# Performance work log

Hardware: AMD Instinct MI355X
Metric: run time of the kernel (lower is better)

The kernel has to match this reference:

```python
import jax, jax.numpy as jnp
import numpy as np

N_NODES = 100000
N_EDGES = 1600000
F_IN = 128
HEADS1, CH1 = 8, 16
N_CLASSES = 64
NEG_SLOPE = 0.2  # PyG GATConv default leaky-relu slope


def setup_inputs() -> dict:
    key = jax.random.key(0)
    ks = jax.random.split(key, 10)
    x = jax.random.normal(ks[0], (N_NODES, F_IN), dtype=jnp.float32)
    edge_index = jax.random.randint(ks[1], (2, N_EDGES), 0, N_NODES, dtype=jnp.int32)
    s1 = 1.0 / np.sqrt(F_IN)
    s2 = 1.0 / np.sqrt(HEADS1 * CH1)
    W1 = jax.random.normal(ks[2], (F_IN, HEADS1 * CH1), dtype=jnp.float32) * s1
    a_src1 = jax.random.normal(ks[3], (HEADS1, CH1), dtype=jnp.float32) * s2
    a_dst1 = jax.random.normal(ks[4], (HEADS1, CH1), dtype=jnp.float32) * s2
    b1 = jnp.zeros((HEADS1 * CH1,), dtype=jnp.float32)
    W2 = jax.random.normal(ks[5], (HEADS1 * CH1, N_CLASSES), dtype=jnp.float32) * s2
    a_src2 = jax.random.normal(ks[6], (1, N_CLASSES), dtype=jnp.float32) * 0.1
    a_dst2 = jax.random.normal(ks[7], (1, N_CLASSES), dtype=jnp.float32) * 0.1
    b2 = jnp.zeros((N_CLASSES,), dtype=jnp.float32)
    return {"x": x, "edge_index": edge_index, "W1": W1, "a_src1": a_src1,
            "a_dst1": a_dst1, "b1": b1, "W2": W2, "a_src2": a_src2,
            "a_dst2": a_dst2, "b2": b2}


def gat_layer(x, src, dst, W, a_src, a_dst, b, heads, ch, concat):
    # PyG GATConv (eval mode, self-loops already appended to src/dst).
    N = x.shape[0]
    h = (x @ W).reshape(N, heads, ch)                      # [N,H,C]
    asn = jnp.einsum('nhc,hc->nh', h, a_src)               # src attention term
    adn = jnp.einsum('nhc,hc->nh', h, a_dst)               # dst attention term
    e = jax.nn.leaky_relu(asn[src] + adn[dst], NEG_SLOPE)  # [E,H]
    emax = jax.ops.segment_max(e, dst, num_segments=N)     # per-dst max (self-loops guarantee nonempty)
    ee = jnp.exp(e - emax[dst])
    denom = jax.ops.segment_sum(ee, dst, num_segments=N)
    alpha = ee / denom[dst]                                # segment softmax over incoming edges
    msg = h[src] * alpha[:, :, None]                       # [E,H,C]
    out = jax.ops.segment_sum(msg, dst, num_segments=N)    # [N,H,C]
    out = out.reshape(N, heads * ch) if concat else out.mean(axis=1)
    return out + b


def reference(x, edge_index, W1, a_src1, a_dst1, b1, W2, a_src2, a_dst2, b2):
    N = x.shape[0]
    loop = jnp.arange(N, dtype=edge_index.dtype)
    src = jnp.concatenate([edge_index[0], loop])  # add self-loops (PyG default)
    dst = jnp.concatenate([edge_index[1], loop])
    h = gat_layer(x, src, dst, W1, a_src1, a_dst1, b1, HEADS1, CH1, True)
    h = jax.nn.elu(h)
    # F.dropout with training=False is identity (eval mode)
    out = gat_layer(h, src, dst, W2, a_src2, a_dst2, b2, 1, N_CLASSES, False)
    return jax.nn.log_softmax(out, axis=1)
```

## Files before the change

kernel.cpp:

```cpp
#include <hip/hip_runtime.h>

#define NN 100000
#define NE 1600000
#define EN (NE + NN)
#define FIN 128
#define H1 8
#define C1 16
#define F1 128
#define NC 64
#define NEG 0.2f

#define BSH 9
#define BKN 512
#define NBUK ((NN + BKN - 1) / BKN)
#define NBLK 256
#define CHUNK ((EN + NBLK - 1) / NBLK)

typedef unsigned short ushort_t;
typedef unsigned int uint_t;
typedef __attribute__((ext_vector_type(8))) short short8v;
typedef __attribute__((ext_vector_type(4))) float f32x4;
typedef __attribute__((ext_vector_type(2))) float f32x2;

union U8 { ushort_t u[8]; short8v v; uint4 q; };

__device__ __forceinline__ ushort_t f2bf(float f) {
  uint_t u = __builtin_bit_cast(uint_t, f);
  u += 0x7FFF + ((u >> 16) & 1);
  return (ushort_t)(u >> 16);
}
__device__ __forceinline__ float bflo(uint_t u) {
  return __builtin_bit_cast(float, u << 16);
}
__device__ __forceinline__ float bfhi(uint_t u) {
  return __builtin_bit_cast(float, u & 0xFFFF0000u);
}

#if __has_builtin(__builtin_amdgcn_cvt_pk_fp8_f32) && \
    __has_builtin(__builtin_amdgcn_cvt_pk_f32_fp8)
__device__ __forceinline__ uint_t fp8_pack4(float f0, float f1, float f2,
                                            float f3) {
  int p = 0;
  p = __builtin_amdgcn_cvt_pk_fp8_f32(f0, f1, p, false);
  p = __builtin_amdgcn_cvt_pk_fp8_f32(f2, f3, p, true);
  return (uint_t)p;
}
__device__ __forceinline__ void fp8_unpack4(uint_t w, float* o) {
  f32x2 d0 = __builtin_amdgcn_cvt_pk_f32_fp8((int)w, false);
  f32x2 d1 = __builtin_amdgcn_cvt_pk_f32_fp8((int)w, true);
  o[0] = d0.x; o[1] = d0.y; o[2] = d1.x; o[3] = d1.y;
}
#else
__device__ __forceinline__ uint_t fp8_enc1(float f) {
  uint_t u = __builtin_bit_cast(uint_t, f);
  uint_t s = (u >> 24) & 0x80u;
  int e = (int)((u >> 23) & 0xFF) - 127;
  if (e < -9) return s;
  if (e < -6) {
    float af = __builtin_bit_cast(float, u & 0x7FFFFFFFu);
    uint_t m = (uint_t)(af * 512.f + 0.5f);
    return s | m;
  }
  uint_t mant = u & 0x7FFFFF;
  uint_t keep = mant >> 20;
  uint_t rest = mant & 0xFFFFF;
  keep += (rest > 0x80000u) || (rest == 0x80000u && (keep & 1));
  uint_t ee = (uint_t)(e + 7);
  if (keep == 8) { keep = 0; ee += 1; }
  if (ee > 15 || (ee == 15 && keep > 6)) return s | 0x7E;
  return s | (ee << 3) | keep;
}
__device__ __forceinline__ float fp8_dec1(uint_t b) {
  uint_t s = (b & 0x80u) << 24;
  uint_t e = (b >> 3) & 15u, m = b & 7u;
  if (e == 0) {
    float v = (float)m * (1.0f / 512.0f);
    return __builtin_bit_cast(float, s | __builtin_bit_cast(uint_t, v));
  }
  return __builtin_bit_cast(float, s | ((e + 120u) << 23) | (m << 20));
}
__device__ __forceinline__ uint_t fp8_pack4(float f0, float f1, float f2,
                                            float f3) {
  return fp8_enc1(f0) | (fp8_enc1(f1) << 8) | (fp8_enc1(f2) << 16) |
         (fp8_enc1(f3) << 24);
}
__device__ __forceinline__ void fp8_unpack4(uint_t w, float* o) {
  o[0] = fp8_dec1(w & 0xFF); o[1] = fp8_dec1((w >> 8) & 0xFF);
  o[2] = fp8_dec1((w >> 16) & 0xFF); o[3] = fp8_dec1(w >> 24);
}
#endif

__global__ __launch_bounds__(256) void mfma_gemm1_kernel(
    const float* __restrict__ X, const ushort_t* __restrict__ WT1,
    const float* __restrict__ a_src, const float* __restrict__ a_dst,
    uint2* __restrict__ h8, float* __restrict__ asn, float* __restrict__ adn,
    int nrows) {
  const int tid = threadIdx.x;
  const int wave = tid >> 6, lane = tid & 63;
  const int row0 = blockIdx.x * 64 + wave * 16;
  const int rlo = lane & 15, khi = lane >> 4;

  f32x4 acc[8];
#pragma unroll
  for (int n = 0; n < 8; ++n) acc[n] = (f32x4){0.f, 0.f, 0.f, 0.f};

#pragma unroll
  for (int ks = 0; ks < 4; ++ks) {
    const int kk = ks * 32 + khi * 8;
    int row = row0 + rlo;
    if (row >= nrows) row = nrows - 1;
    const float4* xp = (const float4*)(X + (size_t)row * 128 + kk);
    float4 u = xp[0], v = xp[1];
    U8 t;
    t.u[0] = f2bf(u.x); t.u[1] = f2bf(u.y); t.u[2] = f2bf(u.z); t.u[3] = f2bf(u.w);
    t.u[4] = f2bf(v.x); t.u[5] = f2bf(v.y); t.u[6] = f2bf(v.z); t.u[7] = f2bf(v.w);
    short8v a = t.v;
#pragma unroll
    for (int nf = 0; nf < 8; ++nf) {
      short8v b = *(const short8v*)(WT1 + (nf * 16 + rlo) * 128 + kk);
      acc[nf] = __builtin_amdgcn_mfma_f32_16x16x32_bf16(a, b, acc[nf], 0, 0, 0);
    }
  }
  const float4* as4 = (const float4*)a_src;
  const float4* ad4 = (const float4*)a_dst;
  float4 as0 = as4[rlo * 2], as1 = as4[rlo * 2 + 1];
  float4 ad0 = ad4[rlo * 2], ad1 = ad4[rlo * 2 + 1];
  int rbase = row0 + khi * 4;
#pragma unroll
  for (int r = 0; r < 4; ++r) {
    int row = rbase + r;
    bool ok = (row < nrows);
    uint2 pk;
    pk.x = fp8_pack4(acc[0][r], acc[1][r], acc[2][r], acc[3][r]);
    pk.y = fp8_pack4(acc[4][r], acc[5][r], acc[6][r], acc[7][r]);
    if (ok) h8[(size_t)row * 16 + rlo] = pk;
    float s = acc[0][r] * as0.x + acc[1][r] * as0.y +
              acc[2][r] * as0.z + acc[3][r] * as0.w +
              acc[4][r] * as1.x + acc[5][r] * as1.y +
              acc[6][r] * as1.z + acc[7][r] * as1.w;
    float d = acc[0][r] * ad0.x + acc[1][r] * ad0.y +
              acc[2][r] * ad0.z + acc[3][r] * ad0.w +
              acc[4][r] * ad1.x + acc[5][r] * ad1.y +
              acc[6][r] * ad1.z + acc[7][r] * ad1.w;
    s += __shfl_xor(s, 1);
    d += __shfl_xor(d, 1);
    if (ok && (rlo & 1) == 0) {
      asn[row * 8 + (rlo >> 1)] = s;
      adn[row * 8 + (rlo >> 1)] = d;
    }
  }
}

__global__ __launch_bounds__(256) void mfma_gemm2_kernel(
    const ushort_t* __restrict__ X2, const ushort_t* __restrict__ WT2,
    const float* __restrict__ a_src, const float* __restrict__ a_dst,
    uint_t* __restrict__ h28, float* __restrict__ asn, float* __restrict__ adn,
    int nrows) {
  const int tid = threadIdx.x;
  const int wave = tid >> 6, lane = tid & 63;
  const int row0 = blockIdx.x * 64 + wave * 16;
  const int rlo = lane & 15, khi = lane >> 4;

  f32x4 acc[4];
#pragma unroll
  for (int n = 0; n < 4; ++n) acc[n] = (f32x4){0.f, 0.f, 0.f, 0.f};

#pragma unroll
  for (int ks = 0; ks < 4; ++ks) {
    const int kk = ks * 32 + khi * 8;
    int row = row0 + rlo;
    if (row >= nrows) row = nrows - 1;
    U8 t;
    t.q = *(const uint4*)(X2 + (size_t)row * 128 + kk);
    short8v a = t.v;
#pragma unroll
    for (int nf = 0; nf < 4; ++nf) {
      short8v b = *(const short8v*)(WT2 + (nf * 16 + rlo) * 128 + kk);
      acc[nf] = __builtin_amdgcn_mfma_f32_16x16x32_bf16(a, b, acc[nf], 0, 0, 0);
    }
  }
  float4 as = ((const float4*)a_src)[rlo];
  float4 ad = ((const float4*)a_dst)[rlo];
  int rbase = row0 + khi * 4;
#pragma unroll
  for (int r = 0; r < 4; ++r) {
    int row = rbase + r;
    bool ok = (row < nrows);
    uint_t pk = fp8_pack4(acc[0][r], acc[1][r], acc[2][r], acc[3][r]);
    if (ok) h28[(size_t)row * 16 + rlo] = pk;
    float s = acc[0][r] * as.x + acc[1][r] * as.y +
              acc[2][r] * as.z + acc[3][r] * as.w;
    float d = acc[0][r] * ad.x + acc[1][r] * ad.y +
              acc[2][r] * ad.z + acc[3][r] * ad.w;
    s += __shfl_xor(s, 1); s += __shfl_xor(s, 2);
    s += __shfl_xor(s, 4); s += __shfl_xor(s, 8);
    d += __shfl_xor(d, 1); d += __shfl_xor(d, 2);
    d += __shfl_xor(d, 4); d += __shfl_xor(d, 8);
    if (ok && rlo == 0) { asn[row] = s; adn[row] = d; }
  }
}

__global__ __launch_bounds__(512) void bucket_count_kernel(
    const int* __restrict__ dstA, int* __restrict__ cnt,
    const float* __restrict__ W1, const float* __restrict__ W2,
    ushort_t* __restrict__ WT1, ushort_t* __restrict__ WT2) {
  __shared__ int histL[NBUK];
  int b = blockIdx.x, t = threadIdx.x;
  int gid = b * 512 + t;
  if (gid < 128 * 128) {
    int n = gid >> 7, k = gid & 127;
    int c = (n & 15) * 8 + (n >> 4);
    WT1[gid] = f2bf(W1[k * 128 + c]);
  } else if (gid < 128 * 128 + 64 * 128) {
    int j = gid - 128 * 128;
    int n = j >> 7, k = j & 127;
    int c = (n & 15) * 4 + (n >> 4);
    WT2[j] = f2bf(W2[k * 64 + c]);
  }
  for (int i = t; i < NBUK; i += 512) histL[i] = 0;
  __syncthreads();
  int e0 = b * CHUNK, e1 = min(e0 + CHUNK, EN);
  for (int e = e0 + t; e < e1; e += 512) {
    int d = (e < NE) ? dstA[e] : (e - NE);
    atomicAdd(&histL[d >> BSH], 1);
  }
  __syncthreads();
  for (int i = t; i < NBUK; i += 512) cnt[i * NBLK + b] = histL[i];
}

__global__ __launch_bounds__(256) void bucket_scan_kernel(
    int* __restrict__ cnt, int* __restrict__ bucket_base) {
  __shared__ int colsum[NBUK];
  int t = threadIdx.x;
  if (t < NBUK) {
    int run = 0;
    int* c = cnt + t * NBLK;
    for (int b = 0; b < NBLK; ++b) { int v = c[b]; c[b] = run; run += v; }
    colsum[t] = run;
  }
  __syncthreads();
  if (t == 0) {
    int base = 0;
    for (int j = 0; j < NBUK; ++j) {
      bucket_base[j] = base;
      int v = colsum[j];
      colsum[j] = base;
      base += v;
    }
    bucket_base[NBUK] = base;
  }
  __syncthreads();
  if (t < NBUK) {
    int bb = colsum[t];
    int* c = cnt + t * NBLK;
    for (int b = 0; b < NBLK; ++b) c[b] += bb;
  }
}

__global__ __launch_bounds__(512) void bucket_scatter_kernel(
    const int* __restrict__ srcA, const int* __restrict__ dstA,
    const int* __restrict__ cnt, int* __restrict__ staging) {
  __shared__ int cur[NBUK];
  int b = blockIdx.x, t = threadIdx.x;
  for (int i = t; i < NBUK; i += 512) cur[i] = cnt[i * NBLK + b];
  __syncthreads();
  int e0 = b * CHUNK, e1 = min(e0 + CHUNK, EN);
  for (int e = e0 + t; e < e1; e += 512) {
    int s, d;
    if (e < NE) { s = srcA[e]; d = dstA[e]; } else { s = e - NE; d = s; }
    int pos = atomicAdd(&cur[d >> BSH], 1);
    staging[pos] = s | ((d & (BKN - 1)) << 17);
  }
}

__global__ __launch_bounds__(512) void bucket_csr_kernel(
    const int* __restrict__ staging, const int* __restrict__ bucket_base,
    int* __restrict__ rp, int* __restrict__ col) {
  __shared__ int degL[BKN];
  __shared__ int exclL[BKN];
  __shared__ int sdata[2][BKN];
  int bk = blockIdx.x, t = threadIdx.x;
  int ebase = bucket_base[bk], eend = bucket_base[bk + 1];
  int ecnt = eend - ebase;
  degL[t] = 0;
  __syncthreads();
  for (int e = t; e < ecnt; e += 512)
    atomicAdd(&degL[staging[ebase + e] >> 17], 1);
  __syncthreads();
  int v = degL[t];
  sdata[0][t] = v;
  __syncthreads();
  int sp = 0;
  for (int off = 1; off < BKN; off <<= 1) {
    int val = sdata[sp][t];
    if (t >= off) val += sdata[sp][t - off];
    sdata[sp ^ 1][t] = val;
    __syncthreads();
    sp ^= 1;
  }
  int ex = sdata[sp][t] - v;
  exclL[t] = ex;
  int node = bk * BKN + t;
  if (node < NN) rp[node] = ebase + ex;
  if (bk == 0 && t == 0) rp[NN] = EN;
  __syncthreads();
  for (int e = t; e < ecnt; e += 512) {
    int pk = staging[ebase + e];
    int pos = atomicAdd(&exclL[pk >> 17], 1);
    col[ebase + pos] = pk & 0x1FFFF;
  }
}

__global__ __launch_bounds__(256) void gather1_kernel(
    const int* __restrict__ rp, const int* __restrict__ col,
    const float* __restrict__ asn, const float* __restrict__ adn,
    const uint4* __restrict__ h8, const float* __restrict__ b1,
    ushort_t* __restrict__ x2) {
  int node = (blockIdx.x << 5) + (threadIdx.x >> 3);
  if (node >= NN) return;
  int lane = threadIdx.x & 7;
  float aD = adn[node * 8 + lane];
  int p = rp[node], p1 = rp[node + 1];
  float a[16];
#pragma unroll
  for (int j = 0; j < 16; ++j) a[j] = 0.f;
  float den = 0.f;

  for (; p + 1 < p1; p += 2) {
    int s0 = col[p], s1 = col[p + 1];
    float e0 = asn[s0 * 8 + lane] + aD;
    float e1 = asn[s1 * 8 + lane] + aD;
    uint4 q0 = h8[(size_t)s0 * 8 + lane];
    uint4 q1 = h8[(size_t)s1 * 8 + lane];
    e0 = e0 > 0.f ? e0 : NEG * e0;
    e1 = e1 > 0.f ? e1 : NEG * e1;
    float ee0 = __expf(e0), ee1 = __expf(e1);
    float d0[4], d1[4], d2[4], d3[4];
    fp8_unpack4(q0.x, d0); fp8_unpack4(q0.y, d1);
    fp8_unpack4(q0.z, d2); fp8_unpack4(q0.w, d3);
    float g0[4], g1[4], g2[4], g3[4];
    fp8_unpack4(q1.x, g0); fp8_unpack4(q1.y, g1);
    fp8_unpack4(q1.z, g2); fp8_unpack4(q1.w, g3);
#pragma unroll
    for (int j = 0; j < 4; ++j) {
      a[j]      += ee0 * d0[j] + ee1 * g0[j];
      a[4 + j]  += ee0 * d1[j] + ee1 * g1[j];
      a[8 + j]  += ee0 * d2[j] + ee1 * g2[j];
      a[12 + j] += ee0 * d3[j] + ee1 * g3[j];
    }
    den += ee0 + ee1;
  }
  if (p < p1) {
    int s0 = col[p];
    float e0 = asn[s0 * 8 + lane] + aD;
    uint4 q0 = h8[(size_t)s0 * 8 + lane];
    e0 = e0 > 0.f ? e0 : NEG * e0;
    float ee0 = __expf(e0);
    float d0[4], d1[4], d2[4], d3[4];
    fp8_unpack4(q0.x, d0); fp8_unpack4(q0.y, d1);
    fp8_unpack4(q0.z, d2); fp8_unpack4(q0.w, d3);
#pragma unroll
    for (int j = 0; j < 4; ++j) {
      a[j] += ee0 * d0[j];
      a[4 + j] += ee0 * d1[j];
      a[8 + j] += ee0 * d2[j];
      a[12 + j] += ee0 * d3[j];
    }
    den += ee0;
  }
  float inv = 1.f / den;
  const float4* b4 = (const float4*)b1;
  U8 t0, t1;
#pragma unroll
  for (int h = 0; h < 4; ++h) {
    float4 bv = b4[lane * 4 + h];
    float o0 = fmaf(a[h * 4 + 0], inv, bv.x);
    float o1 = fmaf(a[h * 4 + 1], inv, bv.y);
    float o2 = fmaf(a[h * 4 + 2], inv, bv.z);
    float o3 = fmaf(a[h * 4 + 3], inv, bv.w);
    o0 = o0 > 0.f ? o0 : __expf(o0) - 1.f;
    o1 = o1 > 0.f ? o1 : __expf(o1) - 1.f;
    o2 = o2 > 0.f ? o2 : __expf(o2) - 1.f;
    o3 = o3 > 0.f ? o3 : __expf(o3) - 1.f;
    U8& t = (h < 2) ? t0 : t1;
    int base = (h & 1) * 4;
    t.u[base + 0] = f2bf(o0); t.u[base + 1] = f2bf(o1);
    t.u[base + 2] = f2bf(o2); t.u[base + 3] = f2bf(o3);
  }
  uint4* xr = (uint4*)(x2 + (size_t)node * F1);
  xr[lane * 2 + 0] = t0.q;
  xr[lane * 2 + 1] = t1.q;
}

__global__ __launch_bounds__(256) void gather2_kernel(
    const int* __restrict__ rp, const int* __restrict__ col,
    const float* __restrict__ asn, const float* __restrict__ adn,
    const uint2* __restrict__ h28, const float* __restrict__ b2,
    float* __restrict__ out) {
  int node = (blockIdx.x << 5) + (threadIdx.x >> 3);
  if (node >= NN) return;
  int lane = threadIdx.x & 7;
  float aD = adn[node];
  int p = rp[node], p1 = rp[node + 1];
  float a[8];
#pragma unroll
  for (int j = 0; j < 8; ++j) a[j] = 0.f;
  float den = 0.f;

  for (; p + 1 < p1; p += 2) {
    int s0 = col[p], s1 = col[p + 1];
    float e0 = asn[s0] + aD;
    float e1 = asn[s1] + aD;
    uint2 q0 = h28[(size_t)s0 * 8 + lane];
    uint2 q1 = h28[(size_t)s1 * 8 + lane];
    e0 = e0 > 0.f ? e0 : NEG * e0;
    e1 = e1 > 0.f ? e1 : NEG * e1;
    float ee0 = __expf(e0), ee1 = __expf(e1);
    float d0[4], d1[4], g0[4], g1[4];
    fp8_unpack4(q0.x, d0); fp8_unpack4(q0.y, d1);
    fp8_unpack4(q1.x, g0); fp8_unpack4(q1.y, g1);
#pragma unroll
    for (int j = 0; j < 4; ++j) {
      a[j] += ee0 * d0[j] + ee1 * g0[j];
      a[4 + j] += ee0 * d1[j] + ee1 * g1[j];
    }
    den += ee0 + ee1;
  }
  if (p < p1) {
    int s0 = col[p];
    float e0 = asn[s0] + aD;
    uint2 q0 = h28[(size_t)s0 * 8 + lane];
    e0 = e0 > 0.f ? e0 : NEG * e0;
    float ee0 = __expf(e0);
    float d0[4], d1[4];
    fp8_unpack4(q0.x, d0); fp8_unpack4(q0.y, d1);
#pragma unroll
    for (int j = 0; j < 4; ++j) {
      a[j] += ee0 * d0[j];
      a[4 + j] += ee0 * d1[j];
    }
    den += ee0;
  }
  float inv = 1.f / den;
  float4 bv0 = ((const float4*)b2)[lane * 2 + 0];
  float4 bv1 = ((const float4*)b2)[lane * 2 + 1];
  float v[8];
  v[0] = fmaf(a[0], inv, bv0.x); v[1] = fmaf(a[1], inv, bv0.y);
  v[2] = fmaf(a[2], inv, bv0.z); v[3] = fmaf(a[3], inv, bv0.w);
  v[4] = fmaf(a[4], inv, bv1.x); v[5] = fmaf(a[5], inv, bv1.y);
  v[6] = fmaf(a[6], inv, bv1.z); v[7] = fmaf(a[7], inv, bv1.w);
  float m = v[0];
#pragma unroll
  for (int j = 1; j < 8; ++j) m = fmaxf(m, v[j]);
#pragma unroll
  for (int k = 1; k < 8; k <<= 1) m = fmaxf(m, __shfl_xor(m, k));
  float ex = 0.f;
#pragma unroll
  for (int j = 0; j < 8; ++j) ex += __expf(v[j] - m);
#pragma unroll
  for (int k = 1; k < 8; k <<= 1) ex += __shfl_xor(ex, k);
  float lse = m + __logf(ex);
  float4 r0 = {v[0] - lse, v[1] - lse, v[2] - lse, v[3] - lse};
  float4 r1 = {v[4] - lse, v[5] - lse, v[6] - lse, v[7] - lse};
  float4* orow = (float4*)(out + (size_t)node * NC);
  orow[lane * 2 + 0] = r0;
  orow[lane * 2 + 1] = r1;
}

extern "C" void kernel_launch(void* const* d_in, const int* in_sizes, int n_in,
                              void* d_out, int out_size, void* d_ws,
                              size_t ws_size, hipStream_t stream) {
  const float* x = (const float*)d_in[0];
  const int* edge_index = (const int*)d_in[1];
  const float* W1 = (const float*)d_in[2];
  const float* a_src1 = (const float*)d_in[3];
  const float* a_dst1 = (const float*)d_in[4];
  const float* b1 = (const float*)d_in[5];
  const float* W2 = (const float*)d_in[6];
  const float* a_src2 = (const float*)d_in[7];
  const float* a_dst2 = (const float*)d_in[8];
  const float* b2 = (const float*)d_in[9];
  float* out = (float*)d_out;
  float* ws = (float*)d_ws;

  ushort_t* x2b = (ushort_t*)ws;
  uint4* h8 = (uint4*)(ws + 6400000);
  uint2* h28 = (uint2*)(ws + 9600000);
  float* asn1 = ws + 11200000;
  float* adn1 = ws + 12000000;
  float* asn2 = ws + 12800000;
  float* adn2 = ws + 12900000;
  ushort_t* WT1 = (ushort_t*)(ws + 13000000);
  ushort_t* WT2 = (ushort_t*)(ws + 13010000);
  int* rp = (int*)(ws + 13020000);
  int* col = rp + NN + 1;
  int* staging = col + EN;
  int* cnt = staging + EN;
  int* bucket_base = cnt + NBUK * NBLK;

  const int* srcA = edge_index;
  const int* dstA = edge_index + NE;

  bucket_count_kernel<<<NBLK, 512, 0, stream>>>(dstA, cnt, W1, W2, WT1, WT2);
  bucket_scan_kernel<<<1, 256, 0, stream>>>(cnt, bucket_base);
  bucket_scatter_kernel<<<NBLK, 512, 0, stream>>>(srcA, dstA, cnt, staging);
  bucket_csr_kernel<<<NBUK, 512, 0, stream>>>(staging, bucket_base, rp, col);

  mfma_gemm1_kernel<<<(NN + 63) / 64, 256, 0, stream>>>(
      x, WT1, a_src1, a_dst1, (uint2*)h8, asn1, adn1, NN);
  gather1_kernel<<<(NN + 31) / 32, 256, 0, stream>>>(rp, col, asn1, adn1, h8,
                                                     b1, x2b);
  mfma_gemm2_kernel<<<(NN + 63) / 64, 256, 0, stream>>>(
      x2b, WT2, a_src2, a_dst2, (uint_t*)h28, asn2, adn2, NN);
  gather2_kernel<<<(NN + 31) / 32, 256, 0, stream>>>(rp, col, asn2, adn2, h28,
                                                     b2, out);
}
```

Before: 217.9 us.

## Fuse edge scatter with first GEMM and unroll gather loops by four

Merges the bucket scatter and the first MFMA GEMM into one launch: the first NBLK blocks do the edge scatter and the rest run GEMM1, now with 512 threads and 128 rows per block. The two independent stages can then overlap on the GPU and one launch is removed. Both gather kernels are also unrolled from 2 to 4 edges per iteration, with all loads issued before the math to expose more memory-level parallelism. This costs more registers per thread, and the GEMM tail block depends on the existing row clamping being correct.

```diff
diff --git a/kernel.cpp b/kernel.cpp
--- a/kernel.cpp
+++ b/kernel.cpp
@@ -90,14 +90,87 @@
 }
 #endif
 
-__global__ __launch_bounds__(256) void mfma_gemm1_kernel(
+__global__ __launch_bounds__(512) void bucket_count_kernel(
+    const int* __restrict__ dstA, int* __restrict__ cnt,
+    const float* __restrict__ W1, const float* __restrict__ W2,
+    ushort_t* __restrict__ WT1, ushort_t* __restrict__ WT2) {
+  __shared__ int histL[NBUK];
+  int b = blockIdx.x, t = threadIdx.x;
+  int gid = b * 512 + t;
+  if (gid < 128 * 128) {
+    int n = gid >> 7, k = gid & 127;
+    int c = (n & 15) * 8 + (n >> 4);
+    WT1[gid] = f2bf(W1[k * 128 + c]);
+  } else if (gid < 128 * 128 + 64 * 128) {
+    int j = gid - 128 * 128;
+    int n = j >> 7, k = j & 127;
+    int c = (n & 15) * 4 + (n >> 4);
+    WT2[j] = f2bf(W2[k * 64 + c]);
+  }
+  for (int i = t; i < NBUK; i += 512) histL[i] = 0;
+  __syncthreads();
+  int e0 = b * CHUNK, e1 = min(e0 + CHUNK, EN);
+  for (int e = e0 + t; e < e1; e += 512) {
+    int d = (e < NE) ? dstA[e] : (e - NE);
+    atomicAdd(&histL[d >> BSH], 1);
+  }
+  __syncthreads();
+  for (int i = t; i < NBUK; i += 512) cnt[i * NBLK + b] = histL[i];
+}
+
+__global__ __launch_bounds__(256) void bucket_scan_kernel(
+    int* __restrict__ cnt, int* __restrict__ bucket_base) {
+  __shared__ int colsum[NBUK];
+  int t = threadIdx.x;
+  if (t < NBUK) {
+    int run = 0;
+    int* c = cnt + t * NBLK;
+    for (int b = 0; b < NBLK; ++b) { int v = c[b]; c[b] = run; run += v; }
+    colsum[t] = run;
+  }
+  __syncthreads();
+  if (t == 0) {
+    int base = 0;
+    for (int j = 0; j < NBUK; ++j) {
+      bucket_base[j] = base;
+      int v = colsum[j];
+      colsum[j] = base;
+      base += v;
+    }
+    bucket_base[NBUK] = base;
+  }
+  __syncthreads();
+  if (t < NBUK) {
+    int bb = colsum[t];
+    int* c = cnt + t * NBLK;
+    for (int b = 0; b < NBLK; ++b) c[b] += bb;
+  }
+}
+
+__global__ __launch_bounds__(512) void scatter_gemm1_kernel(
+    const int* __restrict__ srcA, const int* __restrict__ dstA,
+    const int* __restrict__ cnt, int* __restrict__ staging,
     const float* __restrict__ X, const ushort_t* __restrict__ WT1,
     const float* __restrict__ a_src, const float* __restrict__ a_dst,
     uint2* __restrict__ h8, float* __restrict__ asn, float* __restrict__ adn,
     int nrows) {
+  __shared__ int cur[NBUK];
+  if (blockIdx.x < NBLK) {
+    int b = blockIdx.x, t = threadIdx.x;
+    for (int i = t; i < NBUK; i += 512) cur[i] = cnt[i * NBLK + b];
+    __syncthreads();
+    int e0 = b * CHUNK, e1 = min(e0 + CHUNK, EN);
+    for (int e = e0 + t; e < e1; e += 512) {
+      int s, d;
+      if (e < NE) { s = srcA[e]; d = dstA[e]; } else { s = e - NE; d = s; }
+      int pos = atomicAdd(&cur[d >> BSH], 1);
+      staging[pos] = s | ((d & (BKN - 1)) << 17);
+    }
+    return;
+  }
   const int tid = threadIdx.x;
   const int wave = tid >> 6, lane = tid & 63;
-  const int row0 = blockIdx.x * 64 + wave * 16;
+  const int row0 = (blockIdx.x - NBLK) * 128 + wave * 16;
   const int rlo = lane & 15, khi = lane >> 4;
 
   f32x4 acc[8];
@@ -151,6 +224,44 @@
   }
 }
 
+__global__ __launch_bounds__(512) void bucket_csr_kernel(
+    const int* __restrict__ staging, const int* __restrict__ bucket_base,
+    int* __restrict__ rp, int* __restrict__ col) {
+  __shared__ int degL[BKN];
+  __shared__ int exclL[BKN];
+  __shared__ int sdata[2][BKN];
+  int bk = blockIdx.x, t = threadIdx.x;
+  int ebase = bucket_base[bk], eend = bucket_base[bk + 1];
+  int ecnt = eend - ebase;
+  degL[t] = 0;
+  __syncthreads();
+  for (int e = t; e < ecnt; e += 512)
+    atomicAdd(&degL[staging[ebase + e] >> 17], 1);
+  __syncthreads();
+  int v = degL[t];
+  sdata[0][t] = v;
+  __syncthreads();
+  int sp = 0;
+  for (int off = 1; off < BKN; off <<= 1) {
+    int val = sdata[sp][t];
+    if (t >= off) val += sdata[sp][t - off];
+    sdata[sp ^ 1][t] = val;
+    __syncthreads();
+    sp ^= 1;
+  }
+  int ex = sdata[sp][t] - v;
+  exclL[t] = ex;
+  int node = bk * BKN + t;
+  if (node < NN) rp[node] = ebase + ex;
+  if (bk == 0 && t == 0) rp[NN] = EN;
+  __syncthreads();
+  for (int e = t; e < ecnt; e += 512) {
+    int pk = staging[ebase + e];
+    int pos = atomicAdd(&exclL[pk >> 17], 1);
+    col[ebase + pos] = pk & 0x1FFFF;
+  }
+}
+
 __global__ __launch_bounds__(256) void mfma_gemm2_kernel(
     const ushort_t* __restrict__ X2, const ushort_t* __restrict__ WT2,
     const float* __restrict__ a_src, const float* __restrict__ a_dst,
@@ -200,117 +311,6 @@
   }
 }
 
-__global__ __launch_bounds__(512) void bucket_count_kernel(
-    const int* __restrict__ dstA, int* __restrict__ cnt,
-    const float* __restrict__ W1, const float* __restrict__ W2,
-    ushort_t* __restrict__ WT1, ushort_t* __restrict__ WT2) {
-  __shared__ int histL[NBUK];
-  int b = blockIdx.x, t = threadIdx.x;
-  int gid = b * 512 + t;
-  if (gid < 128 * 128) {
-    int n = gid >> 7, k = gid & 127;
-    int c = (n & 15) * 8 + (n >> 4);
-    WT1[gid] = f2bf(W1[k * 128 + c]);
-  } else if (gid < 128 * 128 + 64 * 128) {
-    int j = gid - 128 * 128;
-    int n = j >> 7, k = j & 127;
-    int c = (n & 15) * 4 + (n >> 4);
-    WT2[j] = f2bf(W2[k * 64 + c]);
-  }
-  for (int i = t; i < NBUK; i += 512) histL[i] = 0;
-  __syncthreads();
-  int e0 = b * CHUNK, e1 = min(e0 + CHUNK, EN);
-  for (int e = e0 + t; e < e1; e += 512) {
-    int d = (e < NE) ? dstA[e] : (e - NE);
-    atomicAdd(&histL[d >> BSH], 1);
-  }
-  __syncthreads();
-  for (int i = t; i < NBUK; i += 512) cnt[i * NBLK + b] = histL[i];
-}
-
-__global__ __launch_bounds__(256) void bucket_scan_kernel(
-    int* __restrict__ cnt, int* __restrict__ bucket_base) {
-  __shared__ int colsum[NBUK];
-  int t = threadIdx.x;
-  if (t < NBUK) {
-    int run = 0;
-    int* c = cnt + t * NBLK;
-    for (int b = 0; b < NBLK; ++b) { int v = c[b]; c[b] = run; run += v; }
-    colsum[t] = run;
-  }
-  __syncthreads();
-  if (t == 0) {
-    int base = 0;
-    for (int j = 0; j < NBUK; ++j) {
-      bucket_base[j] = base;
-      int v = colsum[j];
-      colsum[j] = base;
-      base += v;
-    }
-    bucket_base[NBUK] = base;
-  }
-  __syncthreads();
-  if (t < NBUK) {
-    int bb = colsum[t];
-    int* c = cnt + t * NBLK;
-    for (int b = 0; b < NBLK; ++b) c[b] += bb;
-  }
-}
-
-__global__ __launch_bounds__(512) void bucket_scatter_kernel(
-    const int* __restrict__ srcA, const int* __restrict__ dstA,
-    const int* __restrict__ cnt, int* __restrict__ staging) {
-  __shared__ int cur[NBUK];
-  int b = blockIdx.x, t = threadIdx.x;
-  for (int i = t; i < NBUK; i += 512) cur[i] = cnt[i * NBLK + b];
-  __syncthreads();
-  int e0 = b * CHUNK, e1 = min(e0 + CHUNK, EN);
-  for (int e = e0 + t; e < e1; e += 512) {
-    int s, d;
-    if (e < NE) { s = srcA[e]; d = dstA[e]; } else { s = e - NE; d = s; }
-    int pos = atomicAdd(&cur[d >> BSH], 1);
-    staging[pos] = s | ((d & (BKN - 1)) << 17);
-  }
-}
-
-__global__ __launch_bounds__(512) void bucket_csr_kernel(
-    const int* __restrict__ staging, const int* __restrict__ bucket_base,
-    int* __restrict__ rp, int* __restrict__ col) {
-  __shared__ int degL[BKN];
-  __shared__ int exclL[BKN];
-  __shared__ int sdata[2][BKN];
-  int bk = blockIdx.x, t = threadIdx.x;
-  int ebase = bucket_base[bk], eend = bucket_base[bk + 1];
-  int ecnt = eend - ebase;
-  degL[t] = 0;
-  __syncthreads();
-  for (int e = t; e < ecnt; e += 512)
-    atomicAdd(&degL[staging[ebase + e] >> 17], 1);
-  __syncthreads();
-  int v = degL[t];
-  sdata[0][t] = v;
-  __syncthreads();
-  int sp = 0;
-  for (int off = 1; off < BKN; off <<= 1) {
-    int val = sdata[sp][t];
-    if (t >= off) val += sdata[sp][t - off];
-    sdata[sp ^ 1][t] = val;
-    __syncthreads();
-    sp ^= 1;
-  }
-  int ex = sdata[sp][t] - v;
-  exclL[t] = ex;
-  int node = bk * BKN + t;
-  if (node < NN) rp[node] = ebase + ex;
-  if (bk == 0 && t == 0) rp[NN] = EN;
-  __syncthreads();
-  for (int e = t; e < ecnt; e += 512) {
-    int pk = staging[ebase + e];
-    int pos = atomicAdd(&exclL[pk >> 17], 1);
-    col[ebase + pos] = pk & 0x1FFFF;
-  }
-}
-
 __global__ __launch_bounds__(256) void gather1_kernel(
     const int* __restrict__ rp, const int* __restrict__ col,
     const float* __restrict__ asn, const float* __restrict__ adn,
@@ -326,31 +326,36 @@
   for (int j = 0; j < 16; ++j) a[j] = 0.f;
   float den = 0.f;
 
-  for (; p + 1 < p1; p += 2) {
-    int s0 = col[p], s1 = col[p + 1];
-    float e0 = asn[s0 * 8 + lane] + aD;
-    float e1 = asn[s1 * 8 + lane] + aD;
-    uint4 q0 = h8[(size_t)s0 * 8 + lane];
-    uint4 q1 = h8[(size_t)s1 * 8 + lane];
-    e0 = e0 > 0.f ? e0 : NEG * e0;
-    e1 = e1 > 0.f ? e1 : NEG * e1;
-    float ee0 = __expf(e0), ee1 = __expf(e1);
-    float d0[4], d1[4], d2[4], d3[4];
-    fp8_unpack4(q0.x, d0); fp8_unpack4(q0.y, d1);
-    fp8_unpack4(q0.z, d2); fp8_unpack4(q0.w, d3);
-    float g0[4], g1[4], g2[4], g3[4];
-    fp8_unpack4(q1.x, g0); fp8_unpack4(q1.y, g1);
-    fp8_unpack4(q1.z, g2); fp8_unpack4(q1.w, g3);
-#pragma unroll
-    for (int j = 0; j < 4; ++j) {
-      a[j]      += ee0 * d0[j] + ee1 * g0[j];
-      a[4 + j]  += ee0 * d1[j] + ee1 * g1[j];
-      a[8 + j]  += ee0 * d2[j] + ee1 * g2[j];
-      a[12 + j] += ee0 * d3[j] + ee1 * g3[j];
-    }
-    den += ee0 + ee1;
-  }
-  if (p < p1) {
+  for (; p + 3 < p1; p += 4) {
+    int s[4];
+    uint4 q[4];
+    float e[4];
+#pragma unroll
+    for (int i = 0; i < 4; ++i) s[i] = col[p + i];
+#pragma unroll
+    for (int i = 0; i < 4; ++i) q[i] = h8[(size_t)s[i] * 8 + lane];
+#pragma unroll
+    for (int i = 0; i < 4; ++i) {
+      float t = asn[s[i] * 8 + lane] + aD;
+      t = t > 0.f ? t : NEG * t;
+      e[i] = __expf(t);
+      den += e[i];
+    }
+#pragma unroll
+    for (int i = 0; i < 4; ++i) {
+      float d0[4], d1[4], d2[4], d3[4];
+      fp8_unpack4(q[i].x, d0); fp8_unpack4(q[i].y, d1);
+      fp8_unpack4(q[i].z, d2); fp8_unpack4(q[i].w, d3);
+#pragma unroll
+      for (int j = 0; j < 4; ++j) {
+        a[j]      += e[i] * d0[j];
+        a[4 + j]  += e[i] * d1[j];
+        a[8 + j]  += e[i] * d2[j];
+        a[12 + j] += e[i] * d3[j];
+      }
+    }
+  }
+  for (; p < p1; ++p) {
     int s0 = col[p];
     float e0 = asn[s0 * 8 + lane] + aD;
     uint4 q0 = h8[(size_t)s0 * 8 + lane];
@@ -407,26 +412,33 @@
   for (int j = 0; j < 8; ++j) a[j] = 0.f;
   float den = 0.f;
 
-  for (; p + 1 < p1; p += 2) {
-    int s0 = col[p], s1 = col[p + 1];
-    float e0 = asn[s0] + aD;
-    float e1 = asn[s1] + aD;
-    uint2 q0 = h28[(size_t)s0 * 8 + lane];
-    uint2 q1 = h28[(size_t)s1 * 8 + lane];
-    e0 = e0 > 0.f ? e0 : NEG * e0;
-    e1 = e1 > 0.f ? e1 : NEG * e1;
-    float ee0 = __expf(e0), ee1 = __expf(e1);
-    float d0[4], d1[4], g0[4], g1[4];
-    fp8_unpack4(q0.x, d0); fp8_unpack4(q0.y, d1);
-    fp8_unpack4(q1.x, g0); fp8_unpack4(q1.y, g1);
-#pragma unroll
-    for (int j = 0; j < 4; ++j) {
-      a[j] += ee0 * d0[j] + ee1 * g0[j];
-      a[4 + j] += ee0 * d1[j] + ee1 * g1[j];
-    }
-    den += ee0 + ee1;
-  }
-  if (p < p1) {
+  for (; p + 3 < p1; p += 4) {
+    int s[4];
+    uint2 q[4];
+    float e[4];
+#pragma unroll
+    for (int i = 0; i < 4; ++i) s[i] = col[p + i];
+#pragma unroll
+    for (int i = 0; i < 4; ++i) q[i] = h28[(size_t)s[i] * 8 + lane];
+#pragma unroll
+    for (int i = 0; i < 4; ++i) {
+      float t = asn[s[i]] + aD;
+      t = t > 0.f ? t : NEG * t;
+      e[i] = __expf(t);
+      den += e[i];
+    }
+#pragma unroll
+    for (int i = 0; i < 4; ++i) {
+      float d0[4], d1[4];
+      fp8_unpack4(q[i].x, d0); fp8_unpack4(q[i].y, d1);
+#pragma unroll
+      for (int j = 0; j < 4; ++j) {
+        a[j] += e[i] * d0[j];
+        a[4 + j] += e[i] * d1[j];
+      }
+    }
+  }
+  for (; p < p1; ++p) {
     int s0 = col[p];
     float e0 = asn[s0] + aD;
     uint2 q0 = h28[(size_t)s0 * 8 + lane];
@@ -503,11 +515,10 @@
 
   bucket_count_kernel<<<NBLK, 512, 0, stream>>>(dstA, cnt, W1, W2, WT1, WT2);
   bucket_scan_kernel<<<1, 256, 0, stream>>>(cnt, bucket_base);
-  bucket_scatter_kernel<<<NBLK, 512, 0, stream>>>(srcA, dstA, cnt, staging);
+  scatter_gemm1_kernel<<<NBLK + (NN + 127) / 128, 512, 0, stream>>>(
+      srcA, dstA, cnt, staging, x, WT1, a_src1, a_dst1, (uint2*)h8, asn1, adn1,
+      NN);
   bucket_csr_kernel<<<NBUK, 512, 0, stream>>>(staging, bucket_base, rp, col);
-
-  mfma_gemm1_kernel<<<(NN + 63) / 64, 256, 0, stream>>>(
-      x, WT1, a_src1, a_dst1, (uint2*)h8, asn1, adn1, NN);
   gather1_kernel<<<(NN + 31) / 32, 256, 0, stream>>>(rp, col, asn1, adn1, h8,
                                                      b1, x2b);
   mfma_gemm2_kernel<<<(NN + 63) / 64, 256, 0, stream>>>(
```

After: 219.6 us. About the same (+0.8%).
